# Kernel tuning notes

Hardware: AMD Instinct MI355X
Metric: run time of the kernel (lower is better)

Reference implementation:

```python
import jax, jax.numpy as jnp
import numpy as np

B, T, S, D, H, HD, DFF, NB = 2, 2048, 2048, 768, 12, 64, 3072, 32
HID = H * HD
EPS = 1e-6
NEG = -1e9


def rmsnorm(x, w):
    # T5 RMSNorm: no mean subtraction, no bias
    var = jnp.mean(jnp.square(x), axis=-1, keepdims=True)
    return x * jax.lax.rsqrt(var + EPS) * w


def sdpa(h, kv, m, wq, wk, wv, wo):
    # h: [B,Tq,D], kv: [B,Tk,D], m: additive mask broadcastable to [B,H,Tq,Tk]
    b, tq, _ = h.shape
    tk = kv.shape[1]
    q = (h @ wq).reshape(b, tq, H, HD)
    k = (kv @ wk).reshape(b, tk, H, HD)
    v = (kv @ wv).reshape(b, tk, H, HD)
    scores = jnp.einsum('bthd,bshd->bhts', q, k) + m  # scale=1.0 (T5)
    p = jax.nn.softmax(scores, axis=-1)
    y = jnp.einsum('bhts,bshd->bthd', p, v).reshape(b, tq, HID)
    return y @ wo


def setup_inputs() -> dict:
    key = jax.random.key(0)
    ks = jax.random.split(key, 16)
    x = jax.random.normal(ks[0], (B, T, D), dtype=jnp.float32)
    # causal additive mask for decoder self-attention
    causal = jnp.tril(jnp.ones((T, T), dtype=bool))
    mask = jnp.broadcast_to(jnp.where(causal, 0.0, NEG)[None, None], (B, 1, T, T)).astype(jnp.float32)
    relative_position = jax.random.randint(ks[1], (1, 1, T, T), 0, NB)
    encoder_hidden_states = jax.random.normal(ks[2], (B, S, D), dtype=jnp.float32)
    encoder_attention_mask = jnp.zeros((B, 1, T, S), dtype=jnp.float32)
    sc = 0.02
    p = {
        'sn_w': jnp.ones((D,), jnp.float32),
        'wq': sc * jax.random.normal(ks[3], (D, HID)),
        'wk': sc * jax.random.normal(ks[4], (D, HID)),
        'wv': sc * jax.random.normal(ks[5], (D, HID)),
        'wo': sc * jax.random.normal(ks[6], (HID, D)),
        'rel_emb': sc * jax.random.normal(ks[7], (NB, H)),
        'cn_w': jnp.ones((D,), jnp.float32),
        'cwq': sc * jax.random.normal(ks[8], (D, HID)),
        'cwk': sc * jax.random.normal(ks[9], (D, HID)),
        'cwv': sc * jax.random.normal(ks[10], (D, HID)),
        'cwo': sc * jax.random.normal(ks[11], (HID, D)),
        'pn_w': jnp.ones((D,), jnp.float32),
        'ffn_wi': sc * jax.random.normal(ks[12], (D, DFF)),
        'ffn_wo': sc * jax.random.normal(ks[13], (DFF, D)),
    }
    return dict(x=x, mask=mask, relative_position=relative_position,
                encoder_hidden_states=encoder_hidden_states,
                encoder_attention_mask=encoder_attention_mask, **p)


def reference(x, mask, relative_position, encoder_hidden_states, encoder_attention_mask,
              sn_w, wq, wk, wv, wo, rel_emb, cn_w, cwq, cwk, cwv, cwo, pn_w, ffn_wi, ffn_wo):
    # self-attention with relative-position bias added into additive mask
    h = rmsnorm(x, sn_w)
    # rel_emb[relative_position]: [1,1,T,T,H] -> permute(0,1,4,2,3) -> squeeze(0) -> [1,H,T,T]
    position_bias = jnp.transpose(rel_emb[relative_position], (0, 1, 4, 2, 3))[0]
    self_mask = mask + position_bias
    y = sdpa(h, h, self_mask, wq, wk, wv, wo)
    attn_out = y + x
    # cross-attention (no relative bias -> zeros position bias)
    enc_dec_position_bias = jnp.zeros_like(encoder_attention_mask)
    h2 = rmsnorm(attn_out, cn_w)
    y2 = sdpa(h2, encoder_hidden_states, encoder_attention_mask + enc_dec_position_bias,
              cwq, cwk, cwv, cwo)
    attn_out = y2 + attn_out
    # T5 FFN: relu(x @ wi) @ wo, pre-norm, residual
    hn = rmsnorm(attn_out, pn_w)
    ff = jax.nn.relu(hn @ ffn_wi) @ ffn_wo
    return (attn_out + ff, position_bias, enc_dec_position_bias)
```

## Files before the change

kernel.cpp:

```cpp
#include <hip/hip_runtime.h>
#include <hip/hip_bf16.h>
#include <stdint.h>

#define T5_B   2
#define T5_T   2048
#define T5_S   2048
#define T5_D   768
#define T5_H   12
#define T5_HD  64
#define T5_DFF 3072
#define T5_NB  32
#define NROW   4096

typedef __attribute__((ext_vector_type(8))) short bf16x8;
typedef __attribute__((ext_vector_type(4))) short short4v;
typedef __attribute__((ext_vector_type(4))) float f32x4;

__device__ __forceinline__ unsigned short f2bf(float x) {
  unsigned int u = __float_as_uint(x);
  unsigned int r = (u + 0x7FFFu + ((u >> 16) & 1u)) >> 16;
  return (unsigned short)r;
}

__device__ __forceinline__ void load_lds16(const void* g, void* l) {
  __builtin_amdgcn_global_load_lds(
      (__attribute__((address_space(1))) void*)(const_cast<void*>(g)),
      (__attribute__((address_space(3))) void*)(l), 16, 0, 0);
}

__device__ __forceinline__ unsigned cvt_pk_bf16(float lo_, float hi_) {
  unsigned d;
  asm("v_cvt_pk_bf16_f32 %0, %1, %2" : "=v"(d) : "v"(lo_), "v"(hi_));
  return d;
}

__device__ __forceinline__ f32x4 mfma16(short4v a, short4v b, f32x4 c) {
#if __has_builtin(__builtin_amdgcn_mfma_f32_16x16x16bf16_1k)
  return __builtin_amdgcn_mfma_f32_16x16x16bf16_1k(a, b, c, 0, 0, 0);
#else
  asm volatile("v_mfma_f32_16x16x16_bf16 %0, %1, %2, %0" : "+v"(c) : "v"(a), "v"(b));
  return c;
#endif
}

__device__ __forceinline__ int xcd_swz(int f, int nwg) {
  int q8 = nwg >> 3, r8 = nwg & 7, xcd = f & 7, base = f >> 3;
  return (xcd < r8 ? xcd * (q8 + 1) : r8 * (q8 + 1) + (xcd - r8) * q8) + base;
}

template <int TM, int TN, int EPI>
__device__ __forceinline__ void gemm_body(
    int f, int gx, int nwg,
    const unsigned short* __restrict__ A, const unsigned short* __restrict__ Bt,
    void* __restrict__ C, const float* __restrict__ res, int N, int K,
    unsigned short* LDS) {
  constexpr int WR = (TM >= 128) ? 2 : 1;
  constexpr int WC = 4 / WR;
  constexpr int AM = TM / WR / 16;
  constexpr int AN = TN / WC / 16;
  constexpr int CHA = TM / 8, CHB = TN / 8, CPW = (CHA + CHB) / 4;
  constexpr int BUFSH = (TM + TN) * 64;
  const int tid = threadIdx.x, lane = tid & 63, wv = tid >> 6;
  const int lo = lane & 15, hi = lane >> 4;
  const int wr = wv / WC, wc = wv % WC;
  const int wg = xcd_swz(f, nwg);
  const int m0 = (wg / gx) * TM, n0 = (wg % gx) * TN;

  f32x4 acc[AM][AN];
#pragma unroll
  for (int i = 0; i < AM; ++i)
#pragma unroll
    for (int j = 0; j < AN; ++j) acc[i][j] = f32x4{0.f, 0.f, 0.f, 0.f};

  const int srr  = lane >> 3;
  const int scol = ((lane & 7) ^ srr) * 8;

  auto stage = [&](int k0, int bsel) {
    unsigned short* Ab = LDS + bsel * BUFSH;
    unsigned short* Bb = Ab + TM * 64;
#pragma unroll
    for (int j = 0; j < CPW; ++j) {
      int c = wv * CPW + j;
      if (c < CHA)
        load_lds16(A + (size_t)(m0 + c * 8 + srr) * K + k0 + scol, Ab + c * 512);
      else {
        int c2 = c - CHA;
        load_lds16(Bt + (size_t)(n0 + c2 * 8 + srr) * K + k0 + scol, Bb + c2 * 512);
      }
    }
  };

  stage(0, 0);
  const int nIt = K >> 6;
  for (int it = 0; it < nIt; ++it) {
    const int bsel = it & 1;
    if (it + 1 < nIt) {
      stage((it + 1) << 6, bsel ^ 1);
      asm volatile("s_waitcnt vmcnt(%0)" :: "n"(CPW) : "memory");
    } else {
      asm volatile("s_waitcnt vmcnt(0)" ::: "memory");
    }
    __builtin_amdgcn_s_barrier();
    __builtin_amdgcn_sched_barrier(0);
    const unsigned short* Ab = LDS + bsel * BUFSH;
    const unsigned short* Bb = Ab + TM * 64;
#pragma unroll
    for (int kk = 0; kk < 2; ++kk) {
      bf16x8 af[AM], bfr[AN];
#pragma unroll
      for (int i = 0; i < AM; ++i) {
        int row = wr * (AM * 16) + i * 16 + lo;
        unsigned by = (unsigned)(row * 128) + ((unsigned)(((kk * 4 + hi) ^ (row & 7))) << 4);
        af[i] = *(const bf16x8*)((const char*)Ab + by);
      }
#pragma unroll
      for (int j = 0; j < AN; ++j) {
        int row = wc * (AN * 16) + j * 16 + lo;
        unsigned by = (unsigned)(row * 128) + ((unsigned)(((kk * 4 + hi) ^ (row & 7))) << 4);
        bfr[j] = *(const bf16x8*)((const char*)Bb + by);
      }
      __builtin_amdgcn_s_setprio(1);
#pragma unroll
      for (int i = 0; i < AM; ++i)
#pragma unroll
        for (int j = 0; j < AN; ++j)
          acc[i][j] = __builtin_amdgcn_mfma_f32_16x16x32_bf16(af[i], bfr[j], acc[i][j], 0, 0, 0);
      __builtin_amdgcn_s_setprio(0);
    }
    __builtin_amdgcn_sched_barrier(0);
    __builtin_amdgcn_s_barrier();
  }

#pragma unroll
  for (int mi = 0; mi < AM; ++mi)
#pragma unroll
    for (int ni = 0; ni < AN; ++ni) {
      int row = m0 + wr * (AM * 16) + mi * 16 + hi * 4;
      int col = n0 + wc * (AN * 16) + ni * 16 + lo;
#pragma unroll
      for (int r = 0; r < 4; ++r) {
        float v = acc[mi][ni][r];
        size_t idx = (size_t)(row + r) * N + col;
        if (EPI == 0) {
          ((unsigned short*)C)[idx] = f2bf(v);
        } else if (EPI == 1) {
          ((float*)C)[idx] = v + res[idx];
        } else {
          ((unsigned short*)C)[idx] = f2bf(fmaxf(v, 0.0f));
        }
      }
    }
}

template <int TM, int TN, int EPI>
__global__ __launch_bounds__(256)
void gemm_bt(const unsigned short* __restrict__ A, const unsigned short* __restrict__ Bt,
             void* __restrict__ C, const float* __restrict__ res, int N, int K) {
  __shared__ __align__(16) unsigned short LDS[2 * (TM + TN) * 64];
  int f = blockIdx.y * gridDim.x + blockIdx.x;
  gemm_body<TM, TN, EPI>(f, gridDim.x, gridDim.x * gridDim.y, A, Bt, C, res, N, K, LDS);
}

struct PrepArgs {
  const float* wsrc[10];
  unsigned short* wdst[10];
  const float* enc; unsigned short* encb;
  const int* rp; unsigned char* rp8;
  const float* x; const float* snw; unsigned short* normb;
};

__global__ __launch_bounds__(256)
void prep_kernel(PrepArgs a) {
  __shared__ __align__(16) float tile[32][33];
  const int bid = blockIdx.x, tid = threadIdx.x;
  if (bid < 9216) {
    int widx, rem, Kd, Nd;
    if (bid < 4608)      { widx = bid / 576; rem = bid % 576;  Kd = 768;  Nd = 768;  }
    else if (bid < 6912) { widx = 8;         rem = bid - 4608; Kd = 768;  Nd = 3072; }
    else                 { widx = 9;         rem = bid - 6912; Kd = 3072; Nd = 768;  }
    const float* W = a.wsrc[widx];
    unsigned short* Wt = a.wdst[widx];
    int nb = Nd / 32;
    int n0 = (rem % nb) * 32, k0 = (rem / nb) * 32;
    int tx = tid & 31, ty = tid >> 5;
#pragma unroll
    for (int i = 0; i < 32; i += 8)
      tile[ty + i][tx] = W[(size_t)(k0 + ty + i) * Nd + n0 + tx];
    __syncthreads();
#pragma unroll
    for (int i = 0; i < 32; i += 8)
      Wt[(size_t)(n0 + ty + i) * Kd + k0 + tx] = f2bf(tile[tx][ty + i]);
  } else if (bid < 12288) {
    int i = (bid - 9216) * 256 + tid;
    float4 v = ((const float4*)a.enc)[i];
    unsigned long long pk = (unsigned long long)f2bf(v.x)
                          | ((unsigned long long)f2bf(v.y) << 16)
                          | ((unsigned long long)f2bf(v.z) << 32)
                          | ((unsigned long long)f2bf(v.w) << 48);
    *(unsigned long long*)(a.encb + (size_t)i * 4) = pk;
  } else if (bid < 13312) {
    int idx = (bid - 12288) * 256 + tid;
    const int4* src = (const int4*)(a.rp + (size_t)idx * 16);
    int4 v0 = src[0], v1 = src[1], v2 = src[2], v3 = src[3];
    uint4 o;
    o.x = (v0.x & 31) | ((v0.y & 31) << 8) | ((v0.z & 31) << 16) | ((v0.w & 31) << 24);
    o.y = (v1.x & 31) | ((v1.y & 31) << 8) | ((v1.z & 31) << 16) | ((v1.w & 31) << 24);
    o.z = (v2.x & 31) | ((v2.y & 31) << 8) | ((v2.z & 31) << 16) | ((v2.w & 31) << 24);
    o.w = (v3.x & 31) | ((v3.y & 31) << 8) | ((v3.z & 31) << 16) | ((v3.w & 31) << 24);
    ((uint4*)a.rp8)[idx] = o;
  } else {
    int row = bid - 13312;
    const float* r = a.x + (size_t)row * 768;
    float x0 = r[tid], x1 = r[tid + 256], x2 = r[tid + 512];
    float s = x0 * x0 + x1 * x1 + x2 * x2;
#pragma unroll
    for (int off = 32; off > 0; off >>= 1) s += __shfl_xor(s, off);
    float* wsm = &tile[0][0];
    int lane = tid & 63, wvv = tid >> 6;
    if (lane == 0) wsm[wvv] = s;
    __syncthreads();
    float tot = wsm[0] + wsm[1] + wsm[2] + wsm[3];
    float rinv = rsqrtf(tot * (1.0f / 768.0f) + 1e-6f);
    unsigned short* o = a.normb + (size_t)row * 768;
    o[tid]       = f2bf(x0 * rinv * a.snw[tid]);
    o[tid + 256] = f2bf(x1 * rinv * a.snw[tid + 256]);
    o[tid + 512] = f2bf(x2 * rinv * a.snw[tid + 512]);
  }
}

__global__ __launch_bounds__(256)
void rmsnorm_kernel(const float* __restrict__ in, const float* __restrict__ w,
                    unsigned short* __restrict__ out) {
  int row = blockIdx.x, tid = threadIdx.x;
  const float* r = in + (size_t)row * 768;
  float x0 = r[tid], x1 = r[tid + 256], x2 = r[tid + 512];
  float s = x0 * x0 + x1 * x1 + x2 * x2;
#pragma unroll
  for (int off = 32; off > 0; off >>= 1) s += __shfl_xor(s, off);
  __shared__ float ws_[4];
  int lane = tid & 63, wv = tid >> 6;
  if (lane == 0) ws_[wv] = s;
  __syncthreads();
  float tot = ws_[0] + ws_[1] + ws_[2] + ws_[3];
  float rinv = rsqrtf(tot * (1.0f / 768.0f) + 1e-6f);
  unsigned short* o = out + (size_t)row * 768;
  o[tid]       = f2bf(x0 * rinv * w[tid]);
  o[tid + 256] = f2bf(x1 * rinv * w[tid + 256]);
  o[tid + 512] = f2bf(x2 * rinv * w[tid + 512]);
}

struct Stage1Args {
  const unsigned short *normb, *wqkvT, *encb, *wckvT;
  unsigned short *qkv, *ckv;
  const int* rp; const float* rel;
  float *out1, *out2;
};

__global__ __launch_bounds__(256)
void stage1_kernel(Stage1Args a) {
  __shared__ __align__(16) unsigned short LDS[32768];
  const int bid = blockIdx.x, tid = threadIdx.x;
  if (bid < 576) {
    gemm_body<128, 128, 0>(bid, 18, 576, a.normb, a.wqkvT, a.qkv, nullptr, 2304, 768, LDS);
  } else if (bid < 960) {
    gemm_body<128, 128, 0>(bid - 576, 12, 384, a.encb, a.wckvT, a.ckv, nullptr, 1536, 768, LDS);
  } else {
    const int p = bid - 960;
    float* rl = (float*)LDS;
    for (int i = tid; i < 384; i += 256) rl[i] = a.rel[i];
    __syncthreads();
    int t = p >> 1;
    int s = (p & 1) * 1024 + tid * 4;
    int4 nb = *(const int4*)(a.rp + (size_t)t * 2048 + s);
#pragma unroll
    for (int h = 0; h < 12; ++h) {
      float4 v = make_float4(rl[nb.x * 12 + h], rl[nb.y * 12 + h],
                             rl[nb.z * 12 + h], rl[nb.w * 12 + h]);
      *(float4*)(a.out1 + ((size_t)h * 2048 + t) * 2048 + s) = v;
    }
    size_t zbase = ((size_t)p * 256 + tid) * 8;
    float4 z = make_float4(0.f, 0.f, 0.f, 0.f);
    *(float4*)(a.out2 + zbase)     = z;
    *(float4*)(a.out2 + zbase + 4) = z;
  }
}

__global__ __launch_bounds__(256)
void transpose_both_kernel(const unsigned short* __restrict__ v1,
                           const unsigned short* __restrict__ v2,
                           unsigned short* __restrict__ vT1,
                           unsigned short* __restrict__ vT2) {
  __shared__ __align__(16) unsigned short tile[64][72];
  int which = blockIdx.z >> 1, b = blockIdx.z & 1;
  const unsigned short* vin = which ? v2 : v1;
  int stride = which ? 1536 : 2304;
  unsigned short* vT = which ? vT2 : vT1;
  int t0 = blockIdx.x * 64, h = blockIdx.y;
  int tid = threadIdx.x;
  {
    int tl = tid >> 2, d0 = (tid & 3) * 16;
    const unsigned short* src = vin + (size_t)(b * 2048 + t0 + tl) * stride + h * 64 + d0;
    *(bf16x8*)&tile[tl][d0]     = *(const bf16x8*)src;
    *(bf16x8*)&tile[tl][d0 + 8] = *(const bf16x8*)(src + 8);
  }
  __syncthreads();
  {
    int d = tid >> 2, t1 = (tid & 3) * 16;
    unsigned short tmp[16] __attribute__((aligned(16)));
#pragma unroll
    for (int j = 0; j < 16; ++j) tmp[j] = tile[t1 + j][d];
    unsigned short* dst = vT + ((size_t)((b * 12 + h) * 64 + d)) * 2048 + t0 + t1;
    *(bf16x8*)dst       = *(bf16x8*)&tmp[0];
    *(bf16x8*)(dst + 8) = *(bf16x8*)&tmp[8];
  }
}

template <bool SELF>
__device__ __forceinline__ void attn_qcomp(
    const bf16x8& qf0, const bf16x8& qf1, f32x4* Oc, float& m_, float& l_,
    const unsigned char* rt, const float* rel_l, int qrow, bool edge, int s0,
    const unsigned short* Kb, const unsigned short* Vb, int lo, int hi) {
  f32x4 S[4];
  __builtin_amdgcn_s_setprio(1);
#pragma unroll
  for (int ct = 0; ct < 4; ++ct) {
    int krow = ct * 16 + lo;
    unsigned by0 = ((unsigned)(krow * 128 + hi * 16))      ^ ((unsigned)(krow & 7) << 4);
    unsigned by1 = ((unsigned)(krow * 128 + 64 + hi * 16)) ^ ((unsigned)(krow & 7) << 4);
    bf16x8 kf0 = *(const bf16x8*)((const char*)Kb + by0);
    bf16x8 kf1 = *(const bf16x8*)((const char*)Kb + by1);
    f32x4 sa = f32x4{0.f, 0.f, 0.f, 0.f};
    sa = __builtin_amdgcn_mfma_f32_16x16x32_bf16(kf0, qf0, sa, 0, 0, 0);
    sa = __builtin_amdgcn_mfma_f32_16x16x32_bf16(kf1, qf1, sa, 0, 0, 0);
    S[ct] = sa;
  }
  __builtin_amdgcn_s_setprio(0);

  if constexpr (SELF) {
#pragma unroll
    for (int ct = 0; ct < 4; ++ct) {
      unsigned nb4 = *(const unsigned*)&rt[lo * 64 + ct * 16 + hi * 4];
#pragma unroll
      for (int r = 0; r < 4; ++r) {
        int s = s0 + ct * 16 + hi * 4 + r;
        float sc = S[ct][r] + rel_l[(nb4 >> (8 * r)) & 31u];
        if (edge && s > qrow) sc = -1e30f;
        S[ct][r] = sc;
      }
    }
  }

  float tm = S[0][0];
#pragma unroll
  for (int ct = 0; ct < 4; ++ct)
#pragma unroll
    for (int r = 0; r < 4; ++r) tm = fmaxf(tm, S[ct][r]);
  tm = fmaxf(tm, __shfl_xor(tm, 16));
  tm = fmaxf(tm, __shfl_xor(tm, 32));
  float mn = fmaxf(m_, tm);
  float alpha = __expf(m_ - mn);
  float rs = 0.f;
#pragma unroll
  for (int ct = 0; ct < 4; ++ct)
#pragma unroll
    for (int r = 0; r < 4; ++r) { float e = __expf(S[ct][r] - mn); S[ct][r] = e; rs += e; }
  rs += __shfl_xor(rs, 16);
  rs += __shfl_xor(rs, 32);
  l_ = l_ * alpha + rs;
  if (tm > m_) {
#pragma unroll
    for (int dt = 0; dt < 4; ++dt)
#pragma unroll
      for (int r = 0; r < 4; ++r) Oc[dt][r] *= alpha;
  }
  m_ = mn;

  short4v pf[4];
#pragma unroll
  for (int ct = 0; ct < 4; ++ct) {
    union { unsigned u[2]; short4v s; } cv;
    cv.u[0] = cvt_pk_bf16(S[ct][0], S[ct][1]);
    cv.u[1] = cvt_pk_bf16(S[ct][2], S[ct][3]);
    pf[ct] = cv.s;
  }

  __builtin_amdgcn_s_setprio(1);
#pragma unroll
  for (int dt = 0; dt < 4; ++dt) {
    int vrow = dt * 16 + lo;
#pragma unroll
    for (int ct = 0; ct < 4; ++ct) {
      unsigned vb = ((unsigned)(vrow * 128 + ct * 32 + hi * 8)) ^ ((unsigned)(vrow & 7) << 4);
      short4v vf = *(const short4v*)((const char*)Vb + vb);
      Oc[dt] = mfma16(vf, pf[ct], Oc[dt]);
    }
  }
  __builtin_amdgcn_s_setprio(0);
}

__device__ __forceinline__ void attn_store(f32x4* Oc, float l_, unsigned short* yr) {
  float inv = 1.0f / l_;
#pragma unroll
  for (int dt = 0; dt < 4; ++dt) {
    unsigned long long pk = (unsigned long long)f2bf(Oc[dt][0] * inv)
                          | ((unsigned long long)f2bf(Oc[dt][1] * inv) << 16)
                          | ((unsigned long long)f2bf(Oc[dt][2] * inv) << 32)
                          | ((unsigned long long)f2bf(Oc[dt][3] * inv) << 48);
    *(unsigned long long*)(yr + dt * 16) = pk;
  }
}

__global__ __launch_bounds__(256)
void attn_self_kernel(const unsigned short* __restrict__ qp,
                      const unsigned short* __restrict__ kp,
                      const unsigned short* __restrict__ vT,
                      const unsigned char* __restrict__ rp8,
                      const float* __restrict__ rel_emb,
                      unsigned short* __restrict__ yp) {
  __shared__ __align__(16) unsigned short Kls[2][4096];
  __shared__ __align__(16) unsigned short Vls[2][4096];
  __shared__ __align__(16) unsigned char rp8t[2][8192];
  __shared__ float rel_l[32];

  const int tid = threadIdx.x, lane = tid & 63, wv = tid >> 6;
  const int lo = lane & 15, hi = lane >> 4;
  const int wg = xcd_swz(blockIdx.x + 16 * (blockIdx.y + 12 * blockIdx.z), 384);
  const int xq = wg & 15, h = (wg >> 4) % 12, b = (wg >> 4) / 12;
  const int qta = xq, qtb = 31 - xq;
  const int ntiles = qtb + 1;

  if (tid < 32) rel_l[tid] = rel_emb[tid * 12 + h];

  const int qA = qta * 64 + wv * 16 + lo;
  const int qB = qtb * 64 + wv * 16 + lo;
  const unsigned short* qrA = qp + (size_t)(b * T5_T + qA) * 2304 + h * 64 + hi * 8;
  const unsigned short* qrB = qp + (size_t)(b * T5_T + qB) * 2304 + h * 64 + hi * 8;
  const bf16x8 qa0 = *(const bf16x8*)qrA;
  const bf16x8 qa1 = *(const bf16x8*)(qrA + 32);
  const bf16x8 qb0 = *(const bf16x8*)qrB;
  const bf16x8 qb1 = *(const bf16x8*)(qrB + 32);

  f32x4 OA[4], OB[4];
  float mA = -3.0e38f, lA = 0.f, mB = -3.0e38f, lB = 0.f;
#pragma unroll
  for (int i = 0; i < 4; ++i) { OA[i] = f32x4{0.f, 0.f, 0.f, 0.f}; OB[i] = f32x4{0.f, 0.f, 0.f, 0.f}; }

  const int krr = lane >> 3;
  const int kd0 = ((lane & 7) ^ krr) * 8;

  auto stage = [&](int kt, int bsel) {
    const int s0 = kt * 64;
#pragma unroll
    for (int j = 0; j < 2; ++j) {
      int c = wv * 2 + j;
      int rr = c * 8 + krr;
      load_lds16(kp + (size_t)(b * 2048 + s0 + rr) * 2304 + h * 64 + kd0, &Kls[bsel][c * 512]);
      load_lds16(vT + (size_t)((b * 12 + h) * 64 + rr) * 2048 + s0 + kd0,  &Vls[bsel][c * 512]);
    }
    load_lds16(rp8 + (size_t)(qtb * 64 + wv * 16 + (lane >> 2)) * 2048 + s0 + (lane & 3) * 16,
               &rp8t[bsel][4096 + wv * 1024]);
    if (kt <= qta)
      load_lds16(rp8 + (size_t)(qta * 64 + wv * 16 + (lane >> 2)) * 2048 + s0 + (lane & 3) * 16,
                 &rp8t[bsel][wv * 1024]);
  };

  stage(0, 0);

  for (int kt = 0; kt < ntiles; ++kt) {
    const int bsel = kt & 1;
    const int s0 = kt * 64;
    asm volatile("s_waitcnt vmcnt(0)" ::: "memory");
    __syncthreads();
    if (kt + 1 < ntiles) stage(kt + 1, bsel ^ 1);

    const unsigned short* Kb = &Kls[bsel][0];
    const unsigned short* Vb = &Vls[bsel][0];

    if (kt <= qta)
      attn_qcomp<true>(qa0, qa1, OA, mA, lA, &rp8t[bsel][wv * 1024], rel_l, qA,
                       kt == qta, s0, Kb, Vb, lo, hi);
    attn_qcomp<true>(qb0, qb1, OB, mB, lB, &rp8t[bsel][4096 + wv * 1024], rel_l, qB,
                     kt == qtb, s0, Kb, Vb, lo, hi);
  }

#if !__has_builtin(__builtin_amdgcn_mfma_f32_16x16x16bf16_1k)
  asm volatile("s_nop 7\n\ts_nop 7" ::: );
#endif

  attn_store(OA, lA, yp + (size_t)(b * T5_T + qA) * 768 + h * 64 + hi * 4);
  attn_store(OB, lB, yp + (size_t)(b * T5_T + qB) * 768 + h * 64 + hi * 4);
}

__global__ __launch_bounds__(256)
void attn_cross_kernel(const unsigned short* __restrict__ qp,
                       const unsigned short* __restrict__ kp,
                       const unsigned short* __restrict__ vT,
                       unsigned short* __restrict__ yp) {
  __shared__ __align__(16) unsigned short Kls[2][4096];
  __shared__ __align__(16) unsigned short Vls[2][4096];

  const int tid = threadIdx.x, lane = tid & 63, wv = tid >> 6;
  const int lo = lane & 15, hi = lane >> 4;
  const int wg = xcd_swz(blockIdx.x + 32 * (blockIdx.y + 12 * blockIdx.z), 768);
  const int xq = wg & 31, h = (wg >> 5) % 12, b = (wg >> 5) / 12;

  const int q = xq * 64 + wv * 16 + lo;
  const unsigned short* qr = qp + (size_t)(b * T5_T + q) * 768 + h * 64 + hi * 8;
  const bf16x8 qf0 = *(const bf16x8*)qr;
  const bf16x8 qf1 = *(const bf16x8*)(qr + 32);

  f32x4 Oc[4];
  float m_ = -3.0e38f, l_ = 0.f;
#pragma unroll
  for (int i = 0; i < 4; ++i) Oc[i] = f32x4{0.f, 0.f, 0.f, 0.f};

  const int krr = lane >> 3;
  const int kd0 = ((lane & 7) ^ krr) * 8;

  auto stage = [&](int kt, int bsel) {
    const int s0 = kt * 64;
#pragma unroll
    for (int j = 0; j < 2; ++j) {
      int c = wv * 2 + j;
      int rr = c * 8 + krr;
      load_lds16(kp + (size_t)(b * 2048 + s0 + rr) * 1536 + h * 64 + kd0, &Kls[bsel][c * 512]);
      load_lds16(vT + (size_t)((b * 12 + h) * 64 + rr) * 2048 + s0 + kd0, &Vls[bsel][c * 512]);
    }
  };

  stage(0, 0);

  for (int kt = 0; kt < 32; ++kt) {
    const int bsel = kt & 1;
    asm volatile("s_waitcnt vmcnt(0)" ::: "memory");
    __syncthreads();
    if (kt + 1 < 32) stage(kt + 1, bsel ^ 1);
    attn_qcomp<false>(qf0, qf1, Oc, m_, l_, nullptr, nullptr, 0, false, kt * 64,
                      &Kls[bsel][0], &Vls[bsel][0], lo, hi);
  }

#if !__has_builtin(__builtin_amdgcn_mfma_f32_16x16x16bf16_1k)
  asm volatile("s_nop 7\n\ts_nop 7" ::: );
#endif

  attn_store(Oc, l_, yp + (size_t)(b * T5_T + q) * 768 + h * 64 + hi * 4);
}

extern "C" void kernel_launch(void* const* d_in, const int* in_sizes, int n_in,
                              void* d_out, int out_size, void* d_ws, size_t ws_size,
                              hipStream_t stream) {
  (void)in_sizes; (void)n_in; (void)out_size; (void)ws_size;
  const float* x    = (const float*)d_in[0];
  const int*   rp   = (const int*)d_in[2];
  const float* enc  = (const float*)d_in[3];
  const float* sn_w = (const float*)d_in[5];
  const float* wq   = (const float*)d_in[6];
  const float* wk   = (const float*)d_in[7];
  const float* wvw  = (const float*)d_in[8];
  const float* wo   = (const float*)d_in[9];
  const float* rel  = (const float*)d_in[10];
  const float* cn_w = (const float*)d_in[11];
  const float* cwq  = (const float*)d_in[12];
  const float* cwk  = (const float*)d_in[13];
  const float* cwv  = (const float*)d_in[14];
  const float* cwo  = (const float*)d_in[15];
  const float* pn_w = (const float*)d_in[16];
  const float* wi   = (const float*)d_in[17];
  const float* wo2  = (const float*)d_in[18];

  float* out0 = (float*)d_out;
  float* out1 = out0 + (size_t)NROW * T5_D;
  float* out2 = out1 + (size_t)T5_H * T5_T * T5_T;

  char* ws = (char*)d_ws;
  size_t off = 0;
  auto alloc = [&](size_t bytes) { char* p = ws + off; off += (bytes + 255) & ~(size_t)255; return p; };
  unsigned short* wqkvT = (unsigned short*)alloc((size_t)2304 * 768 * 2);
  unsigned short* woT   = (unsigned short*)alloc((size_t)768 * 768 * 2);
  unsigned short* wckvT = (unsigned short*)alloc((size_t)1536 * 768 * 2);
  unsigned short* wcqT  = (unsigned short*)alloc((size_t)768 * 768 * 2);
  unsigned short* wcoT  = (unsigned short*)alloc((size_t)768 * 768 * 2);
  unsigned short* wiT   = (unsigned short*)alloc((size_t)3072 * 768 * 2);
  unsigned short* woT2  = (unsigned short*)alloc((size_t)768 * 3072 * 2);
  unsigned short* normb = (unsigned short*)alloc((size_t)NROW * 768 * 2);
  unsigned short* encb  = (unsigned short*)alloc((size_t)NROW * 768 * 2);
  unsigned short* ybuf  = (unsigned short*)alloc((size_t)NROW * 768 * 2);
  unsigned short* cq    = (unsigned short*)alloc((size_t)NROW * 768 * 2);
  float*          attn  = (float*)alloc((size_t)NROW * 768 * 4);
  unsigned char*  rp8p  = (unsigned char*)alloc((size_t)2048 * 2048);
  unsigned short* qkv   = (unsigned short*)alloc((size_t)NROW * 2304 * 2);
  unsigned short* ckv   = (unsigned short*)alloc((size_t)NROW * 1536 * 2);
  unsigned short* vT1   = (unsigned short*)alloc((size_t)24 * 64 * 2048 * 2);
  unsigned short* vT2   = (unsigned short*)alloc((size_t)24 * 64 * 2048 * 2);
  unsigned short* ffh   = (unsigned short*)alloc((size_t)NROW * 3072 * 2);

  dim3 blk(256);

  {
    PrepArgs pa;
    pa.wsrc[0] = wq;  pa.wdst[0] = wqkvT;
    pa.wsrc[1] = wk;  pa.wdst[1] = wqkvT + 768 * 768;
    pa.wsrc[2] = wvw; pa.wdst[2] = wqkvT + 2 * 768 * 768;
    pa.wsrc[3] = wo;  pa.wdst[3] = woT;
    pa.wsrc[4] = cwk; pa.wdst[4] = wckvT;
    pa.wsrc[5] = cwv; pa.wdst[5] = wckvT + 768 * 768;
    pa.wsrc[6] = cwq; pa.wdst[6] = wcqT;
    pa.wsrc[7] = cwo; pa.wdst[7] = wcoT;
    pa.wsrc[8] = wi;  pa.wdst[8] = wiT;
    pa.wsrc[9] = wo2; pa.wdst[9] = woT2;
    pa.enc = enc; pa.encb = encb; pa.rp = rp; pa.rp8 = rp8p;
    pa.x = x; pa.snw = sn_w; pa.normb = normb;
    prep_kernel<<<17408, blk, 0, stream>>>(pa);
  }

  {
    Stage1Args sa;
    sa.normb = normb; sa.wqkvT = wqkvT; sa.encb = encb; sa.wckvT = wckvT;
    sa.qkv = qkv; sa.ckv = ckv; sa.rp = rp; sa.rel = rel;
    sa.out1 = out1; sa.out2 = out2;
    stage1_kernel<<<5056, blk, 0, stream>>>(sa);
  }

  transpose_both_kernel<<<dim3(32, 12, 4), blk, 0, stream>>>(qkv + 1536, ckv + 768, vT1, vT2);

  attn_self_kernel<<<dim3(16, 12, 2), blk, 0, stream>>>(qkv, qkv + 768, vT1, rp8p, rel, ybuf);
  gemm_bt<64, 64, 1><<<dim3(12, 64), blk, 0, stream>>>(ybuf, woT, attn, x, 768, 768);

  rmsnorm_kernel<<<NROW, blk, 0, stream>>>(attn, cn_w, normb);
  gemm_bt<64, 64, 0><<<dim3(12, 64), blk, 0, stream>>>(normb, wcqT, cq, nullptr, 768, 768);
  attn_cross_kernel<<<dim3(32, 12, 2), blk, 0, stream>>>(cq, ckv, vT2, ybuf);
  gemm_bt<64, 64, 1><<<dim3(12, 64), blk, 0, stream>>>(ybuf, wcoT, attn, attn, 768, 768);

  rmsnorm_kernel<<<NROW, blk, 0, stream>>>(attn, pn_w, normb);
  gemm_bt<128, 128, 2><<<dim3(24, 32), blk, 0, stream>>>(normb, wiT, ffh, nullptr, 3072, 768);
  gemm_bt<64, 64, 1><<<dim3(12, 64), blk, 0, stream>>>(ffh, woT2, out0, attn, 768, 3072);
}
```

Before: 360.8 us.

## Add triple-buffered GEMM pipeline and split self-attention into one q-tile per block

Generalizes the GEMM body to a configurable number of LDS buffers and uses three stages for the 64x64 GEMMs, prefetching two K-tiles ahead to hide global-load latency. The self-attention kernel changes from paired q-tiles per workgroup (a balanced causal pair) to one q-tile per workgroup across twice as many blocks. It also loads relative-position buckets directly from global memory into registers instead of staging them in LDS. This trades causal load balance and LDS reuse for more parallelism and fewer LDS reads. The extra GEMM buffer increases LDS use per block, which may reduce occupancy.

```diff
diff --git a/kernel.cpp b/kernel.cpp
--- a/kernel.cpp
+++ b/kernel.cpp
@@ -48,7 +48,7 @@
   return (xcd < r8 ? xcd * (q8 + 1) : r8 * (q8 + 1) + (xcd - r8) * q8) + base;
 }
 
-template <int TM, int TN, int EPI>
+template <int TM, int TN, int EPI, int NBUF>
 __device__ __forceinline__ void gemm_body(
     int f, int gx, int nwg,
     const unsigned short* __restrict__ A, const unsigned short* __restrict__ Bt,
@@ -60,6 +60,7 @@
   constexpr int AN = TN / WC / 16;
   constexpr int CHA = TM / 8, CHB = TN / 8, CPW = (CHA + CHB) / 4;
   constexpr int BUFSH = (TM + TN) * 64;
+  constexpr int DEPTH = NBUF - 1;
   const int tid = threadIdx.x, lane = tid & 63, wv = tid >> 6;
   const int lo = lane & 15, hi = lane >> 4;
   const int wr = wv / WC, wc = wv % WC;
@@ -90,12 +91,17 @@
     }
   };
 
-  stage(0, 0);
   const int nIt = K >> 6;
+#pragma unroll
+  for (int p = 0; p < DEPTH; ++p)
+    if (p < nIt) stage(p << 6, p % NBUF);
+
   for (int it = 0; it < nIt; ++it) {
-    const int bsel = it & 1;
-    if (it + 1 < nIt) {
-      stage((it + 1) << 6, bsel ^ 1);
+    const int bsel = it % NBUF;
+    if (it + DEPTH < nIt) {
+      stage((it + DEPTH) << 6, (it + DEPTH) % NBUF);
+      asm volatile("s_waitcnt vmcnt(%0)" :: "n"(DEPTH * CPW) : "memory");
+    } else if (it + 1 < nIt) {
       asm volatile("s_waitcnt vmcnt(%0)" :: "n"(CPW) : "memory");
     } else {
       asm volatile("s_waitcnt vmcnt(0)" ::: "memory");
@@ -152,13 +158,13 @@
     }
 }
 
-template <int TM, int TN, int EPI>
+template <int TM, int TN, int EPI, int NBUF>
 __global__ __launch_bounds__(256)
 void gemm_bt(const unsigned short* __restrict__ A, const unsigned short* __restrict__ Bt,
              void* __restrict__ C, const float* __restrict__ res, int N, int K) {
-  __shared__ __align__(16) unsigned short LDS[2 * (TM + TN) * 64];
+  __shared__ __align__(16) unsigned short LDS[NBUF * (TM + TN) * 64];
   int f = blockIdx.y * gridDim.x + blockIdx.x;
-  gemm_body<TM, TN, EPI>(f, gridDim.x, gridDim.x * gridDim.y, A, Bt, C, res, N, K, LDS);
+  gemm_body<TM, TN, EPI, NBUF>(f, gridDim.x, gridDim.x * gridDim.y, A, Bt, C, res, N, K, LDS);
 }
 
 struct PrepArgs {
@@ -261,9 +267,9 @@
   __shared__ __align__(16) unsigned short LDS[32768];
   const int bid = blockIdx.x, tid = threadIdx.x;
   if (bid < 576) {
-    gemm_body<128, 128, 0>(bid, 18, 576, a.normb, a.wqkvT, a.qkv, nullptr, 2304, 768, LDS);
+    gemm_body<128, 128, 0, 2>(bid, 18, 576, a.normb, a.wqkvT, a.qkv, nullptr, 2304, 768, LDS);
   } else if (bid < 960) {
-    gemm_body<128, 128, 0>(bid - 576, 12, 384, a.encb, a.wckvT, a.ckv, nullptr, 1536, 768, LDS);
+    gemm_body<128, 128, 0, 2>(bid - 576, 12, 384, a.encb, a.wckvT, a.ckv, nullptr, 1536, 768, LDS);
   } else {
     const int p = bid - 960;
     float* rl = (float*)LDS;
@@ -318,7 +324,7 @@
 template <bool SELF>
 __device__ __forceinline__ void attn_qcomp(
     const bf16x8& qf0, const bf16x8& qf1, f32x4* Oc, float& m_, float& l_,
-    const unsigned char* rt, const float* rel_l, int qrow, bool edge, int s0,
+    const unsigned* nb4, const float* rel_l, int qrow, bool edge, int s0,
     const unsigned short* Kb, const unsigned short* Vb, int lo, int hi) {
   f32x4 S[4];
   __builtin_amdgcn_s_setprio(1);
@@ -339,11 +345,10 @@
   if constexpr (SELF) {
 #pragma unroll
     for (int ct = 0; ct < 4; ++ct) {
-      unsigned nb4 = *(const unsigned*)&rt[lo * 64 + ct * 16 + hi * 4];
 #pragma unroll
       for (int r = 0; r < 4; ++r) {
         int s = s0 + ct * 16 + hi * 4 + r;
-        float sc = S[ct][r] + rel_l[(nb4 >> (8 * r)) & 31u];
+        float sc = S[ct][r] + rel_l[(nb4[ct] >> (8 * r)) & 31u];
         if (edge && s > qrow) sc = -1e30f;
         S[ct][r] = sc;
       }
@@ -419,31 +424,27 @@
                       unsigned short* __restrict__ yp) {
   __shared__ __align__(16) unsigned short Kls[2][4096];
   __shared__ __align__(16) unsigned short Vls[2][4096];
-  __shared__ __align__(16) unsigned char rp8t[2][8192];
   __shared__ float rel_l[32];
 
   const int tid = threadIdx.x, lane = tid & 63, wv = tid >> 6;
   const int lo = lane & 15, hi = lane >> 4;
-  const int wg = xcd_swz(blockIdx.x + 16 * (blockIdx.y + 12 * blockIdx.z), 384);
-  const int xq = wg & 15, h = (wg >> 4) % 12, b = (wg >> 4) / 12;
-  const int qta = xq, qtb = 31 - xq;
-  const int ntiles = qtb + 1;
+  const int wg = xcd_swz(blockIdx.x + 32 * (blockIdx.y + 12 * blockIdx.z), 768);
+  const int qt = 31 - (wg & 31);
+  const int h = (wg >> 5) % 12, b = (wg >> 5) / 12;
+  const int ntiles = qt + 1;
 
   if (tid < 32) rel_l[tid] = rel_emb[tid * 12 + h];
 
-  const int qA = qta * 64 + wv * 16 + lo;
-  const int qB = qtb * 64 + wv * 16 + lo;
-  const unsigned short* qrA = qp + (size_t)(b * T5_T + qA) * 2304 + h * 64 + hi * 8;
-  const unsigned short* qrB = qp + (size_t)(b * T5_T + qB) * 2304 + h * 64 + hi * 8;
-  const bf16x8 qa0 = *(const bf16x8*)qrA;
-  const bf16x8 qa1 = *(const bf16x8*)(qrA + 32);
-  const bf16x8 qb0 = *(const bf16x8*)qrB;
-  const bf16x8 qb1 = *(const bf16x8*)(qrB + 32);
-
-  f32x4 OA[4], OB[4];
-  float mA = -3.0e38f, lA = 0.f, mB = -3.0e38f, lB = 0.f;
-#pragma unroll
-  for (int i = 0; i < 4; ++i) { OA[i] = f32x4{0.f, 0.f, 0.f, 0.f}; OB[i] = f32x4{0.f, 0.f, 0.f, 0.f}; }
+  const int q = qt * 64 + wv * 16 + lo;
+  const unsigned short* qr = qp + (size_t)(b * T5_T + q) * 2304 + h * 64 + hi * 8;
+  const bf16x8 qf0 = *(const bf16x8*)qr;
+  const bf16x8 qf1 = *(const bf16x8*)(qr + 32);
+  const unsigned char* rpq = rp8 + (size_t)q * 2048 + hi * 4;
+
+  f32x4 Oc[4];
+  float m_ = -3.0e38f, l_ = 0.f;
+#pragma unroll
+  for (int i = 0; i < 4; ++i) Oc[i] = f32x4{0.f, 0.f, 0.f, 0.f};
 
   const int krr = lane >> 3;
   const int kd0 = ((lane & 7) ^ krr) * 8;
@@ -457,11 +458,6 @@
       load_lds16(kp + (size_t)(b * 2048 + s0 + rr) * 2304 + h * 64 + kd0, &Kls[bsel][c * 512]);
       load_lds16(vT + (size_t)((b * 12 + h) * 64 + rr) * 2048 + s0 + kd0,  &Vls[bsel][c * 512]);
     }
-    load_lds16(rp8 + (size_t)(qtb * 64 + wv * 16 + (lane >> 2)) * 2048 + s0 + (lane & 3) * 16,
-               &rp8t[bsel][4096 + wv * 1024]);
-    if (kt <= qta)
-      load_lds16(rp8 + (size_t)(qta * 64 + wv * 16 + (lane >> 2)) * 2048 + s0 + (lane & 3) * 16,
-                 &rp8t[bsel][wv * 1024]);
   };
 
   stage(0, 0);
@@ -471,24 +467,21 @@
     const int s0 = kt * 64;
     asm volatile("s_waitcnt vmcnt(0)" ::: "memory");
     __syncthreads();
+    unsigned nb4[4];
+#pragma unroll
+    for (int ct = 0; ct < 4; ++ct)
+      nb4[ct] = *(const unsigned*)(rpq + s0 + ct * 16);
     if (kt + 1 < ntiles) stage(kt + 1, bsel ^ 1);
 
-    const unsigned short* Kb = &Kls[bsel][0];
-    const unsigned short* Vb = &Vls[bsel][0];
-
-    if (kt <= qta)
-      attn_qcomp<true>(qa0, qa1, OA, mA, lA, &rp8t[bsel][wv * 1024], rel_l, qA,
-                       kt == qta, s0, Kb, Vb, lo, hi);
-    attn_qcomp<true>(qb0, qb1, OB, mB, lB, &rp8t[bsel][4096 + wv * 1024], rel_l, qB,
-                     kt == qtb, s0, Kb, Vb, lo, hi);
+    attn_qcomp<true>(qf0, qf1, Oc, m_, l_, nb4, rel_l, q, kt == qt, s0,
+                     &Kls[bsel][0], &Vls[bsel][0], lo, hi);
   }
 
 #if !__has_builtin(__builtin_amdgcn_mfma_f32_16x16x16bf16_1k)
   asm volatile("s_nop 7\n\ts_nop 7" ::: );
 #endif
 
-  attn_store(OA, lA, yp + (size_t)(b * T5_T + qA) * 768 + h * 64 + hi * 4);
-  attn_store(OB, lB, yp + (size_t)(b * T5_T + qB) * 768 + h * 64 + hi * 4);
+  attn_store(Oc, l_, yp + (size_t)(b * T5_T + q) * 768 + h * 64 + hi * 4);
 }
 
 __global__ __launch_bounds__(256)
@@ -623,15 +616,15 @@
 
   transpose_both_kernel<<<dim3(32, 12, 4), blk, 0, stream>>>(qkv + 1536, ckv + 768, vT1, vT2);
 
-  attn_self_kernel<<<dim3(16, 12, 2), blk, 0, stream>>>(qkv, qkv + 768, vT1, rp8p, rel, ybuf);
-  gemm_bt<64, 64, 1><<<dim3(12, 64), blk, 0, stream>>>(ybuf, woT, attn, x, 768, 768);
+  attn_self_kernel<<<dim3(32, 12, 2), blk, 0, stream>>>(qkv, qkv + 768, vT1, rp8p, rel, ybuf);
+  gemm_bt<64, 64, 1, 3><<<dim3(12, 64), blk, 0, stream>>>(ybuf, woT, attn, x, 768, 768);
 
   rmsnorm_kernel<<<NROW, blk, 0, stream>>>(attn, cn_w, normb);
-  gemm_bt<64, 64, 0><<<dim3(12, 64), blk, 0, stream>>>(normb, wcqT, cq, nullptr, 768, 768);
+  gemm_bt<64, 64, 0, 3><<<dim3(12, 64), blk, 0, stream>>>(normb, wcqT, cq, nullptr, 768, 768);
   attn_cross_kernel<<<dim3(32, 12, 2), blk, 0, stream>>>(cq, ckv, vT2, ybuf);
-  gemm_bt<64, 64, 1><<<dim3(12, 64), blk, 0, stream>>>(ybuf, wcoT, attn, attn, 768, 768);
+  gemm_bt<64, 64, 1, 3><<<dim3(12, 64), blk, 0, stream>>>(ybuf, wcoT, attn, attn, 768, 768);
 
   rmsnorm_kernel<<<NROW, blk, 0, stream>>>(attn, pn_w, normb);
-  gemm_bt<128, 128, 2><<<dim3(24, 32), blk, 0, stream>>>(normb, wiT, ffh, nullptr, 3072, 768);
-  gemm_bt<64, 64, 1><<<dim3(12, 64), blk, 0, stream>>>(ffh, woT2, out0, attn, 768, 3072);
-}
+  gemm_bt<128, 128, 2, 2><<<dim3(24, 32), blk, 0, stream>>>(normb, wiT, ffh, nullptr, 3072, 768);
+  gemm_bt<64, 64, 1, 3><<<dim3(12, 64), blk, 0, stream>>>(ffh, woT2, out0, attn, 768, 3072);
+}
```

Result: no change. 366.1 us (+1.5%).
